# Kernel tuning notes

Hardware: AMD Instinct MI355X
Metric: run time of the kernel (lower is better)

Reference implementation:

```python
import jax, jax.numpy as jnp
import numpy as np

EPS = 1e-3  # Keras BatchNormalization default epsilon


def _bn_params(key, c):
    k1, k2, k3, k4 = jax.random.split(key, 4)
    gamma = 1.0 + 0.1 * jax.random.normal(k1, (c,), jnp.float32)
    beta = 0.1 * jax.random.normal(k2, (c,), jnp.float32)
    mean = 0.1 * jax.random.normal(k3, (c,), jnp.float32)
    var = 0.5 + jax.random.uniform(k4, (c,), jnp.float32)
    return jnp.stack([gamma, beta, mean, var])  # (4, c)


def bn(x, p):
    g, b, m, v = p[0], p[1], p[2], p[3]
    return (x - m) * jax.lax.rsqrt(v + EPS) * g + b


def setup_inputs() -> dict:
    key = jax.random.key(0)
    ks = jax.random.split(key, 32)
    B, N, C, K = 32, 2048, 3, 32
    MLP1, UNITS = 128, 512
    w = lambda k, shp, fan: jax.random.normal(k, shp, jnp.float32) / np.sqrt(fan)
    inp = {
        "inputs": jax.random.normal(ks[0], (B, N, C), jnp.float32),
        "indices": jax.random.randint(ks[1], (B, N, K), 0, N, jnp.int32),
        "t_conv1_w": w(ks[2], (C, 64), C), "t_conv1_b": 0.1 * jax.random.normal(ks[3], (64,), jnp.float32),
        "t_bn1": _bn_params(ks[4], 64),
        "t_dense1_w": w(ks[5], (64, 64), 64), "t_dense1_b": 0.1 * jax.random.normal(ks[6], (64,), jnp.float32),
        "t_bn2": _bn_params(ks[7], 64),
        "t_dense2_w": w(ks[8], (64, C * C), 64), "t_dense2_b": 0.1 * jax.random.normal(ks[9], (C * C,), jnp.float32),
        "conv1_w": w(ks[10], (K * C, MLP1), K * C), "conv1_b": 0.1 * jax.random.normal(ks[11], (MLP1,), jnp.float32),
        "bn1": _bn_params(ks[12], MLP1),
        "conv2_w": w(ks[13], (MLP1, 2 * MLP1), MLP1), "conv2_b": 0.1 * jax.random.normal(ks[14], (2 * MLP1,), jnp.float32),
        "bn2": _bn_params(ks[15], 2 * MLP1),
        "bn3": _bn_params(ks[16], 2 * MLP1),
        "dense1_w": w(ks[17], (2 * MLP1, C), 2 * MLP1), "dense1_b": 0.1 * jax.random.normal(ks[18], (C,), jnp.float32),
        "conv3_w": w(ks[19], (C, UNITS), C), "conv3_b": 0.1 * jax.random.normal(ks[20], (UNITS,), jnp.float32),
        "bn4": _bn_params(ks[21], UNITS),
        "blk1_w": w(ks[22], (UNITS, UNITS // 2), UNITS), "blk1_b": 0.1 * jax.random.normal(ks[23], (UNITS // 2,), jnp.float32),
        "blk1_bn": _bn_params(ks[24], UNITS // 2),
        "blk2_w": w(ks[25], (UNITS // 2, UNITS // 4), UNITS // 2), "blk2_b": 0.1 * jax.random.normal(ks[26], (UNITS // 4,), jnp.float32),
        "blk2_bn": _bn_params(ks[27], UNITS // 4),
        "bn_globf": _bn_params(ks[28], UNITS // 4),
    }
    return inp


def reference(inputs, indices, t_conv1_w, t_conv1_b, t_bn1, t_dense1_w, t_dense1_b,
              t_bn2, t_dense2_w, t_dense2_b, conv1_w, conv1_b, bn1, conv2_w, conv2_b,
              bn2, bn3, dense1_w, dense1_b, conv3_w, conv3_b, bn4,
              blk1_w, blk1_b, blk1_bn, blk2_w, blk2_b, blk2_bn, bn_globf):
    B, N, C = inputs.shape
    # --- TNetLess (inference: dropout = identity) ---
    x = jax.nn.relu(bn(inputs @ t_conv1_w + t_conv1_b, t_bn1))   # (B,N,64)
    x = jnp.max(x, axis=1)                                        # global max pool -> (B,64)
    x = jax.nn.relu(bn(x @ t_dense1_w + t_dense1_b, t_bn2))      # (B,64)
    transform = (x @ t_dense2_w + t_dense2_b).reshape(B, C, C)   # (B,C,C)
    pct = jnp.einsum('bnc,bcd->bnd', inputs, transform)          # transformed cloud (B,N,C)
    # --- random neighbor gather (batch_dims=1) ---
    feats = pct[jnp.arange(B)[:, None, None], indices]           # (B,N,K,C)
    feats = feats.reshape(B, N, -1)                               # (B,N,K*C)
    # --- pointwise MLP over gathered neighbor features ---
    feats = jax.nn.relu(bn(feats @ conv1_w + conv1_b, bn1))      # (B,N,128)
    feats = jax.nn.relu(bn(feats @ conv2_w + conv2_b, bn2))      # (B,N,256)
    g = bn(jnp.max(feats, axis=1), bn3)                           # (B,256)
    g = jnp.broadcast_to(g[:, None, :], (B, N, g.shape[-1]))     # tile to (B,N,256)
    g = g @ dense1_w + dense1_b                                   # (B,N,C)
    combined = jnp.concatenate([pct, g], axis=1)                  # concat on point axis -> (B,2N,C)
    # --- conv3 + conv blocks (kernel_size=1 -> pointwise) ---
    net = jax.nn.relu(bn(combined @ conv3_w + conv3_b, bn4))     # (B,2N,512)
    net = jax.nn.relu(bn(net @ blk1_w + blk1_b, blk1_bn))        # (B,2N,256)
    net = jax.nn.relu(bn(net @ blk2_w + blk2_b, blk2_bn))        # (B,2N,128)
    net = jnp.max(net, axis=1)                                    # (B,128)
    return bn(net, bn_globf)
```

## Files before the change

kernel.cpp:

```cpp
#include <hip/hip_runtime.h>

typedef unsigned short u16;
typedef unsigned int u32;
typedef __attribute__((ext_vector_type(8))) short bf16x8;
typedef __attribute__((ext_vector_type(4))) float f32x4;

#define EPSBN 0.001f
#define MFMA16(a, b, c) __builtin_amdgcn_mfma_f32_16x16x32_bf16(a, b, c, 0, 0, 0)

__device__ __forceinline__ float bf2f(u16 u) {
    return __uint_as_float(((u32)u) << 16);
}
__device__ __forceinline__ u16 f2bf(float f) {
    u32 u = __float_as_uint(f);
    u32 r = u + 0x7FFFu + ((u >> 16) & 1u);
    return (u16)(r >> 16);
}
__device__ __forceinline__ float relu(float x) { return x > 0.f ? x : 0.f; }

#define A_INPUTS 64
#define A_TC1W  196672
#define A_TC1B  196864
#define A_TBN1  196928
#define A_TD1W  197184
#define A_TD1B  201280
#define A_TBN2  201344
#define A_TD2W  201600
#define A_TD2B  202176
#define A_C1W   202240
#define A_C1B   214528
#define A_BN1   214656
#define A_C2W   215168
#define A_C2B   247936
#define A_BN2   248192
#define A_BN3   249216
#define A_D1W   250240
#define A_D1B   251008
#define A_C3W   251072
#define A_C3B   252608
#define A_BN4   253120
#define A_BLK1W 255168
#define A_BLK1B 386240
#define A_BLK1BN 386496
#define A_BLK2W 387520
#define A_BLK2B 420288
#define A_BLK2BN 420416
#define A_BNGF  420928
#define S_TRF   423488
#define S_PCT   423808
#define S_MAXF  620544
#define S_NETMAX 628736
#define S_XMAX  632832
#define T_C1WT  634880
#define T_C2WT  641024
#define T_W4T   657408
#define T_W5T   722944

struct ConvArgs {
    const void* src[28];
    int n[28];
    int off[28];
};

struct PrepArgs {
    const float* src[4];
    u16* dst[4];
    int K[4];
    int logN[4];
    int base[4];
};

__global__ __launch_bounds__(256) void k_convert(ConvArgs a, const u16* __restrict__ tbn1,
                                                 float* __restrict__ ws, u32* __restrict__ flag) {
    int ok = 1;
    for (int i = 0; i < 16; i += 2) {
        u16 v = tbn1[i];
        if (v < 0x3E00u || v > 0x4080u) ok = 0;
    }
    if (blockIdx.x == 0 && blockIdx.y == 0 && threadIdx.x == 0) flag[0] = ok ? 1u : 0u;

    int t = blockIdx.y;
    int n = a.n[t];
    int cpb = (n + 31) >> 5;
    int s = blockIdx.x * cpb;
    int e = s + cpb; if (e > n) e = n;
    float* dst = ws + a.off[t];
    if (ok) {
        const u16* src = (const u16*)a.src[t];
        for (int i = s + (int)threadIdx.x; i < e; i += 256) dst[i] = bf2f(src[i]);
    } else {
        const float* src = (const float*)a.src[t];
        for (int i = s + (int)threadIdx.x; i < e; i += 256) dst[i] = src[i];
    }
}

__global__ __launch_bounds__(256) void k_prepw_all(PrepArgs pa) {
    int blk = blockIdx.x;
    int t = (blk < 48) ? 0 : (blk < 176) ? 1 : (blk < 688) ? 2 : 3;
    int i = (blk - pa.base[t]) * 256 + (int)threadIdx.x;
    int N1 = (1 << pa.logN[t]) - 1;
    int k = i >> pa.logN[t], c = i & N1;
    pa.dst[t][c * pa.K[t] + k] = f2bf(pa.src[t][i]);
}

__global__ __launch_bounds__(256) void k_tnet1(const float* __restrict__ inp,
                                               const float* __restrict__ w,
                                               const float* __restrict__ bias,
                                               const float* __restrict__ bn,
                                               u32* __restrict__ xmax) {
    __shared__ float pts[1536];
    __shared__ float wred[4][64];
    int b = blockIdx.y, slice = blockIdx.x, tid = threadIdx.x;
    const float* ip = inp + ((size_t)b * 2048 + slice * 512) * 3;
#pragma unroll
    for (int i = 0; i < 6; i++) pts[tid + i * 256] = ip[tid + i * 256];

    int c = tid & 63, np = tid >> 6;
    float w0 = w[c], w1 = w[64 + c], w2 = w[128 + c], bi = bias[c];
    float g = bn[c], be = bn[64 + c], m = bn[128 + c], v = bn[192 + c];
    float s = g * rsqrtf(v + EPSBN), t = be - m * s;
    __syncthreads();

    float vmax = 0.f;
    int pbase = np * 128;
#pragma unroll 4
    for (int p = 0; p < 128; p++) {
        float x0 = pts[(pbase + p) * 3], x1 = pts[(pbase + p) * 3 + 1], x2 = pts[(pbase + p) * 3 + 2];
        float z = x0 * w0 + x1 * w1 + x2 * w2 + bi;
        vmax = fmaxf(vmax, z * s + t);
    }
    wred[np][c] = vmax;
    __syncthreads();
    if (tid < 64) {
        float mm = fmaxf(fmaxf(wred[0][tid], wred[1][tid]), fmaxf(wred[2][tid], wred[3][tid]));
        atomicMax(&xmax[b * 64 + tid], __float_as_uint(relu(mm)));
    }
}

__global__ __launch_bounds__(64) void k_tnet2(const float* __restrict__ xmax,
                                              const float* __restrict__ w1, const float* __restrict__ b1,
                                              const float* __restrict__ bn2p,
                                              const float* __restrict__ w2, const float* __restrict__ b2,
                                              float* __restrict__ transform) {
    int b = blockIdx.x, t = threadIdx.x;
    __shared__ float x2[64];
    const float* xm = xmax + b * 64;
    float acc = b1[t];
    for (int j = 0; j < 64; j++) acc += xm[j] * w1[j * 64 + t];
    float g = bn2p[t], be = bn2p[64 + t], m = bn2p[128 + t], v = bn2p[192 + t];
    float s = g * rsqrtf(v + EPSBN);
    x2[t] = relu(acc * s + (be - m * s));
    __syncthreads();
    if (t < 9) {
        float a = b2[t];
        for (int j = 0; j < 64; j++) a += x2[j] * w2[j * 9 + t];
        transform[b * 9 + t] = a;
    }
}

__global__ __launch_bounds__(256) void k_pct(const float* __restrict__ inp,
                                             const float* __restrict__ transform,
                                             float* __restrict__ pct) {
    int b = blockIdx.y;
    int n = blockIdx.x * 256 + threadIdx.x;
    __shared__ float T[9];
    if (threadIdx.x < 9) T[threadIdx.x] = transform[b * 9 + threadIdx.x];
    __syncthreads();
    const float* ip = inp + ((size_t)b * 2048 + n) * 3;
    float x0 = ip[0], x1 = ip[1], x2 = ip[2];
    float* op = pct + ((size_t)b * 2049 + n) * 3;
    op[0] = x0 * T[0] + x1 * T[3] + x2 * T[6];
    op[1] = x0 * T[1] + x1 * T[4] + x2 * T[7];
    op[2] = x0 * T[2] + x1 * T[5] + x2 * T[8];
}

__global__ __launch_bounds__(256) void k_feat(const float* __restrict__ pct,
                                              const int* __restrict__ indices,
                                              const u16* __restrict__ w1t, const float* __restrict__ b1,
                                              const float* __restrict__ bn1p,
                                              const u16* __restrict__ w2t, const float* __restrict__ b2,
                                              const float* __restrict__ bn2p,
                                              u32* __restrict__ maxfeats) {
    __shared__ __align__(16) u16 ftA[4096];
    __shared__ __align__(16) u16 h1B[4096];
    __shared__ float sB1[128], sS1[128], sT1[128];
    __shared__ float sB2[256], sS2[256], sT2[256];

    int b = blockIdx.y, n0p = blockIdx.x * 32, tid = threadIdx.x;
    if (tid < 128) {
        float g = bn1p[tid], be = bn1p[128 + tid], m = bn1p[256 + tid], v = bn1p[384 + tid];
        float s = g * rsqrtf(v + EPSBN);
        sS1[tid] = s; sT1[tid] = be - m * s; sB1[tid] = b1[tid];
    }
    {
        int c = tid;
        float g = bn2p[c], be = bn2p[256 + c], m = bn2p[512 + c], v = bn2p[768 + c];
        float s = g * rsqrtf(v + EPSBN);
        sS2[c] = s; sT2[c] = be - m * s; sB2[c] = b2[c];
    }
    {
        const float* pb = pct + (size_t)b * 2049 * 3;
        const int* ib = indices + ((size_t)b * 2048 + n0p) * 32;
        char* fA = (char*)ftA;
#pragma unroll
        for (int r = 0; r < 4; r++) {
            int i = tid + 256 * r;
            int p = i >> 5, k = i & 31;
            int idx = ib[p * 32 + k];
            const float* s = pb + (size_t)idx * 3;
            int sw = (p & 7) << 4;
            int base = p * 256 + 6 * k;
            *(u16*)(fA + ((base) ^ sw)) = f2bf(s[0]);
            *(u16*)(fA + ((base + 2) ^ sw)) = f2bf(s[1]);
            *(u16*)(fA + ((base + 4) ^ sw)) = f2bf(s[2]);
        }
    }
    __syncthreads();

    int lane = tid & 63, wv = tid >> 6;
    int rw = lane & 15, kq = lane >> 4;
    int axor = (rw & 7) << 4;

    {
        f32x4 acc[2][2];
#pragma unroll
        for (int m = 0; m < 2; m++)
#pragma unroll
            for (int n = 0; n < 2; n++) acc[m][n] = (f32x4){0.f, 0.f, 0.f, 0.f};
        const char* fA = (const char*)ftA;
        const char* W = (const char*)w1t;
        int nb = wv * 32;
#pragma unroll
        for (int ks = 0; ks < 3; ks++) {
            bf16x8 a0 = *(const bf16x8*)(fA + ((rw * 256 + ks * 64 + kq * 16) ^ axor));
            bf16x8 a1 = *(const bf16x8*)(fA + (((rw + 16) * 256 + ks * 64 + kq * 16) ^ axor));
            bf16x8 b0 = *(const bf16x8*)(W + ((nb + rw) * 192 + ks * 64 + kq * 16));
            bf16x8 b1v = *(const bf16x8*)(W + ((nb + 16 + rw) * 192 + ks * 64 + kq * 16));
            acc[0][0] = MFMA16(a0, b0, acc[0][0]);
            acc[1][0] = MFMA16(a1, b0, acc[1][0]);
            acc[0][1] = MFMA16(a0, b1v, acc[0][1]);
            acc[1][1] = MFMA16(a1, b1v, acc[1][1]);
        }
        char* hB = (char*)h1B;
#pragma unroll
        for (int nt = 0; nt < 2; nt++) {
            int c = nb + nt * 16 + rw;
            float s = sS1[c], t = sT1[c], bi = sB1[c];
#pragma unroll
            for (int m = 0; m < 2; m++)
#pragma unroll
                for (int r = 0; r < 4; r++) {
                    int rr = m * 16 + kq * 4 + r;
                    float h = relu((acc[m][nt][r] + bi) * s + t);
                    *(u16*)(hB + ((rr * 256 + c * 2) ^ ((rr & 7) << 4))) = f2bf(h);
                }
        }
    }
    __syncthreads();
    {
        f32x4 acc[2][4];
#pragma unroll
        for (int m = 0; m < 2; m++)
#pragma unroll
            for (int n = 0; n < 4; n++) acc[m][n] = (f32x4){0.f, 0.f, 0.f, 0.f};
        const char* hB = (const char*)h1B;
        const char* W = (const char*)w2t;
        int nb = wv * 64;
#pragma unroll
        for (int ks = 0; ks < 4; ks++) {
            bf16x8 a0 = *(const bf16x8*)(hB + ((rw * 256 + ks * 64 + kq * 16) ^ axor));
            bf16x8 a1 = *(const bf16x8*)(hB + (((rw + 16) * 256 + ks * 64 + kq * 16) ^ axor));
#pragma unroll
            for (int nt = 0; nt < 4; nt++) {
                bf16x8 bv = *(const bf16x8*)(W + ((nb + nt * 16 + rw) * 256 + ks * 64 + kq * 16));
                acc[0][nt] = MFMA16(a0, bv, acc[0][nt]);
                acc[1][nt] = MFMA16(a1, bv, acc[1][nt]);
            }
        }
#pragma unroll
        for (int nt = 0; nt < 4; nt++) {
            int c = nb + nt * 16 + rw;
            float s = sS2[c], t = sT2[c], bi = sB2[c];
            float vm = 0.f;
#pragma unroll
            for (int m = 0; m < 2; m++)
#pragma unroll
                for (int r = 0; r < 4; r++)
                    vm = fmaxf(vm, relu((acc[m][nt][r] + bi) * s + t));
            vm = fmaxf(vm, __shfl_xor(vm, 16));
            vm = fmaxf(vm, __shfl_xor(vm, 32));
            if (kq == 0) atomicMax(&maxfeats[b * 256 + c], __float_as_uint(vm));
        }
    }
}

__global__ __launch_bounds__(256) void k_gvec(const u32* __restrict__ maxfeats,
                                              const float* __restrict__ bn3p,
                                              const float* __restrict__ dw, const float* __restrict__ db,
                                              float* __restrict__ pct) {
    int b = blockIdx.x, c = threadIdx.x;
    __shared__ float red[3][256];
    float mf = __uint_as_float(maxfeats[b * 256 + c]);
    float g = bn3p[c], be = bn3p[256 + c], m = bn3p[512 + c], v = bn3p[768 + c];
    float s = g * rsqrtf(v + EPSBN);
    float y = mf * s + (be - m * s);
    red[0][c] = y * dw[c * 3 + 0];
    red[1][c] = y * dw[c * 3 + 1];
    red[2][c] = y * dw[c * 3 + 2];
    __syncthreads();
    for (int st = 128; st > 0; st >>= 1) {
        if (c < st) {
            red[0][c] += red[0][c + st];
            red[1][c] += red[1][c + st];
            red[2][c] += red[2][c + st];
        }
        __syncthreads();
    }
    if (c < 3) pct[((size_t)b * 2049 + 2048) * 3 + c] = red[c][0] + db[c];
}

__global__ __launch_bounds__(256) void k_mlp(const float* __restrict__ pct,
                                             const float* __restrict__ w3, const float* __restrict__ b3,
                                             const float* __restrict__ bn4p,
                                             const u16* __restrict__ w4t, const float* __restrict__ b4f,
                                             const float* __restrict__ bn5p,
                                             const u16* __restrict__ w5t, const float* __restrict__ b5f,
                                             const float* __restrict__ bn6p,
                                             u32* __restrict__ netmax) {
    __shared__ __align__(16) u16 hA[16384];
    __shared__ __align__(16) u16 hB[8192];
    __shared__ float rowsS[128];
    __shared__ float sB4[256], sS5[256], sT5[256];
    __shared__ float sB5[128], sS6[128], sT6[128];

    int b = blockIdx.y, r0 = blockIdx.x * 32, tid = threadIdx.x;
    int nrows = 2049 - r0; if (nrows > 32) nrows = 32;

    {
        int c = tid;
        float g = bn5p[c], be = bn5p[256 + c], m = bn5p[512 + c], v = bn5p[768 + c];
        float s = g * rsqrtf(v + EPSBN);
        sS5[c] = s; sT5[c] = be - m * s; sB4[c] = b4f[c];
    }
    if (tid < 128) {
        int c = tid;
        float g = bn6p[c], be = bn6p[128 + c], m = bn6p[256 + c], v = bn6p[384 + c];
        float s = g * rsqrtf(v + EPSBN);
        sS6[c] = s; sT6[c] = be - m * s; sB5[c] = b5f[c];
    }
    if (tid < 32) {
        float v0 = 0.f, v1 = 0.f, v2 = 0.f;
        if (tid < nrows) {
            const float* s = pct + ((size_t)b * 2049 + r0 + tid) * 3;
            v0 = s[0]; v1 = s[1]; v2 = s[2];
        }
        rowsS[tid * 4] = v0; rowsS[tid * 4 + 1] = v1; rowsS[tid * 4 + 2] = v2;
    }
    __syncthreads();
    {
        char* hAc = (char*)hA;
#pragma unroll
        for (int half = 0; half < 2; half++) {
            int c = tid + half * 256;
            float w0 = w3[c], w1f = w3[512 + c], w2f = w3[1024 + c];
            float bi = b3[c];
            float g = bn4p[c], be = bn4p[512 + c], m = bn4p[1024 + c], v = bn4p[1536 + c];
            float s = g * rsqrtf(v + EPSBN), t = be - m * s;
#pragma unroll
            for (int p = 0; p < 32; p++) {
                float z = rowsS[p * 4] * w0 + rowsS[p * 4 + 1] * w1f + rowsS[p * 4 + 2] * w2f + bi;
                float h = relu(z * s + t);
                *(u16*)(hAc + ((p * 1024 + c * 2) ^ ((p & 7) << 4))) = f2bf(h);
            }
        }
    }
    __syncthreads();

    int lane = tid & 63, wv = tid >> 6;
    int rw = lane & 15, kq = lane >> 4;
    int axor = (rw & 7) << 4;

    {
        f32x4 acc[2][4];
#pragma unroll
        for (int m = 0; m < 2; m++)
#pragma unroll
            for (int n = 0; n < 4; n++) acc[m][n] = (f32x4){0.f, 0.f, 0.f, 0.f};
        const char* A = (const char*)hA;
        const char* W = (const char*)w4t;
        int nb = wv * 64;
        auto lA = [&](int m, int ks) -> bf16x8 {
            return *(const bf16x8*)(A + (((rw + m) * 1024 + ks * 64 + kq * 16) ^ axor));
        };
        auto lB = [&](int nt, int ks) -> bf16x8 {
            return *(const bf16x8*)(W + ((nb + nt * 16 + rw) * 1024 + ks * 64 + kq * 16));
        };
        bf16x8 a0 = lA(0, 0), a1 = lA(16, 0);
        bf16x8 b0 = lB(0, 0), b1v = lB(1, 0), b2v = lB(2, 0), b3v = lB(3, 0);
#pragma unroll
        for (int ks = 0; ks < 16; ks++) {
            bf16x8 na0, na1, nb0, nb1, nb2, nb3;
            if (ks < 15) {
                na0 = lA(0, ks + 1); na1 = lA(16, ks + 1);
                nb0 = lB(0, ks + 1); nb1 = lB(1, ks + 1); nb2 = lB(2, ks + 1); nb3 = lB(3, ks + 1);
            }
            acc[0][0] = MFMA16(a0, b0, acc[0][0]);  acc[1][0] = MFMA16(a1, b0, acc[1][0]);
            acc[0][1] = MFMA16(a0, b1v, acc[0][1]); acc[1][1] = MFMA16(a1, b1v, acc[1][1]);
            acc[0][2] = MFMA16(a0, b2v, acc[0][2]); acc[1][2] = MFMA16(a1, b2v, acc[1][2]);
            acc[0][3] = MFMA16(a0, b3v, acc[0][3]); acc[1][3] = MFMA16(a1, b3v, acc[1][3]);
            if (ks < 15) { a0 = na0; a1 = na1; b0 = nb0; b1v = nb1; b2v = nb2; b3v = nb3; }
        }
        char* HB = (char*)hB;
#pragma unroll
        for (int nt = 0; nt < 4; nt++) {
            int c = nb + nt * 16 + rw;
            float s = sS5[c], t = sT5[c], bi = sB4[c];
#pragma unroll
            for (int m = 0; m < 2; m++)
#pragma unroll
                for (int r = 0; r < 4; r++) {
                    int rr = m * 16 + kq * 4 + r;
                    float h = relu((acc[m][nt][r] + bi) * s + t);
                    *(u16*)(HB + ((rr * 512 + c * 2) ^ ((rr & 7) << 4))) = f2bf(h);
                }
        }
    }
    __syncthreads();
    {
        f32x4 acc[2][2];
#pragma unroll
        for (int m = 0; m < 2; m++)
#pragma unroll
            for (int n = 0; n < 2; n++) acc[m][n] = (f32x4){0.f, 0.f, 0.f, 0.f};
        const char* A = (const char*)hB;
        const char* W = (const char*)w5t;
        int nb = wv * 32;
#pragma unroll
        for (int ks = 0; ks < 8; ks++) {
            bf16x8 a0 = *(const bf16x8*)(A + ((rw * 512 + ks * 64 + kq * 16) ^ axor));
            bf16x8 a1 = *(const bf16x8*)(A + (((rw + 16) * 512 + ks * 64 + kq * 16) ^ axor));
            bf16x8 w0 = *(const bf16x8*)(W + ((nb + rw) * 512 + ks * 64 + kq * 16));
            bf16x8 w1v = *(const bf16x8*)(W + ((nb + 16 + rw) * 512 + ks * 64 + kq * 16));
            acc[0][0] = MFMA16(a0, w0, acc[0][0]);
            acc[1][0] = MFMA16(a1, w0, acc[1][0]);
            acc[0][1] = MFMA16(a0, w1v, acc[0][1]);
            acc[1][1] = MFMA16(a1, w1v, acc[1][1]);
        }
#pragma unroll
        for (int nt = 0; nt < 2; nt++) {
            int c = nb + nt * 16 + rw;
            float s = sS6[c], t = sT6[c], bi = sB5[c];
            float vm = 0.f;
#pragma unroll
            for (int m = 0; m < 2; m++)
#pragma unroll
                for (int r = 0; r < 4; r++) {
                    int rr = m * 16 + kq * 4 + r;
                    float h = relu((acc[m][nt][r] + bi) * s + t);
                    if (rr < nrows) vm = fmaxf(vm, h);
                }
            vm = fmaxf(vm, __shfl_xor(vm, 16));
            vm = fmaxf(vm, __shfl_xor(vm, 32));
            if (kq == 0) atomicMax(&netmax[b * 128 + c], __float_as_uint(vm));
        }
    }
}

__global__ __launch_bounds__(256) void k_out(const u32* __restrict__ netmax,
                                             const float* __restrict__ bng,
                                             const u32* __restrict__ flag,
                                             void* __restrict__ out) {
    int i = blockIdx.x * 256 + threadIdx.x;
    int c = i & 127;
    float v = __uint_as_float(netmax[i]);
    float g = bng[c], be = bng[128 + c], m = bng[256 + c], va = bng[384 + c];
    float s = g * rsqrtf(va + EPSBN);
    float val = v * s + (be - m * s);
    if (flag[0]) ((u16*)out)[i] = f2bf(val);
    else ((float*)out)[i] = val;
}

extern "C" void kernel_launch(void* const* d_in, const int* in_sizes, int n_in,
                              void* d_out, int out_size, void* d_ws, size_t ws_size,
                              hipStream_t stream) {
    float* ws = (float*)d_ws;
    u32* flag = (u32*)ws;

    static const int order[28] = {0,2,3,4,5,6,7,8,9,10,11,12,13,14,15,16,17,18,19,20,21,22,23,24,25,26,27,28};
    static const int nels[28] = {196608,192,64,256,4096,64,256,576,9,12288,128,512,32768,256,1024,1024,768,3,1536,512,2048,131072,256,1024,32768,128,512,512};
    static const int offs[28] = {A_INPUTS,A_TC1W,A_TC1B,A_TBN1,A_TD1W,A_TD1B,A_TBN2,A_TD2W,A_TD2B,A_C1W,A_C1B,A_BN1,A_C2W,A_C2B,A_BN2,A_BN3,A_D1W,A_D1B,A_C3W,A_C3B,A_BN4,A_BLK1W,A_BLK1B,A_BLK1BN,A_BLK2W,A_BLK2B,A_BLK2BN,A_BNGF};
    ConvArgs ca;
    for (int i = 0; i < 28; i++) { ca.src[i] = d_in[order[i]]; ca.n[i] = nels[i]; ca.off[i] = offs[i]; }

    const int* indices = (const int*)d_in[1];

    k_convert<<<dim3(32, 28), 256, 0, stream>>>(ca, (const u16*)d_in[4], ws, flag);

    PrepArgs pa;
    pa.src[0] = ws + A_C1W;   pa.dst[0] = (u16*)(ws + T_C1WT); pa.K[0] = 96;  pa.logN[0] = 7; pa.base[0] = 0;
    pa.src[1] = ws + A_C2W;   pa.dst[1] = (u16*)(ws + T_C2WT); pa.K[1] = 128; pa.logN[1] = 8; pa.base[1] = 48;
    pa.src[2] = ws + A_BLK1W; pa.dst[2] = (u16*)(ws + T_W4T);  pa.K[2] = 512; pa.logN[2] = 8; pa.base[2] = 176;
    pa.src[3] = ws + A_BLK2W; pa.dst[3] = (u16*)(ws + T_W5T);  pa.K[3] = 256; pa.logN[3] = 7; pa.base[3] = 688;
    k_prepw_all<<<816, 256, 0, stream>>>(pa);

    hipMemsetAsync(ws + S_MAXF, 0, (size_t)14336 * 4, stream);

    k_tnet1<<<dim3(4, 32), 256, 0, stream>>>(ws + A_INPUTS, ws + A_TC1W, ws + A_TC1B, ws + A_TBN1,
                                             (u32*)(ws + S_XMAX));
    k_tnet2<<<32, 64, 0, stream>>>((const float*)(ws + S_XMAX), ws + A_TD1W, ws + A_TD1B, ws + A_TBN2,
                                   ws + A_TD2W, ws + A_TD2B, ws + S_TRF);
    k_pct<<<dim3(8, 32), 256, 0, stream>>>(ws + A_INPUTS, ws + S_TRF, ws + S_PCT);
    k_feat<<<dim3(64, 32), 256, 0, stream>>>(ws + S_PCT, indices,
                                             (const u16*)(ws + T_C1WT), ws + A_C1B, ws + A_BN1,
                                             (const u16*)(ws + T_C2WT), ws + A_C2B, ws + A_BN2,
                                             (u32*)(ws + S_MAXF));
    k_gvec<<<32, 256, 0, stream>>>((u32*)(ws + S_MAXF), ws + A_BN3, ws + A_D1W, ws + A_D1B, ws + S_PCT);
    k_mlp<<<dim3(65, 32), 256, 0, stream>>>(ws + S_PCT,
                                            ws + A_C3W, ws + A_C3B, ws + A_BN4,
                                            (const u16*)(ws + T_W4T), ws + A_BLK1B, ws + A_BLK1BN,
                                            (const u16*)(ws + T_W5T), ws + A_BLK2B, ws + A_BLK2BN,
                                            (u32*)(ws + S_NETMAX));
    k_out<<<16, 256, 0, stream>>>((u32*)(ws + S_NETMAX), ws + A_BNGF, flag, d_out);
}
```

Measured before the change: 271.2 us.

## Fold batchnorm into weights and double row tiles with chunked conv3 pipelining

Batchnorm scale and shift are folded into the bf16 weight transposes and the bias vectors during weight prep, so the MLP epilogues become a bias-add plus relu. k_feat and k_mlp now process 64 rows per block instead of 32, which halves the grid and reuses each weight fragment across four M tiles. In k_mlp the conv3 activations are produced in 64-channel chunks into a double buffer, interleaved with the blk1 MFMA loop, which shrinks LDS and overlaps the VALU work with matrix ops. The risks are higher register pressure under launch_bounds(256,3), a barrier per chunk, and a smaller grid.

```diff
diff --git a/kernel.cpp b/kernel.cpp
--- a/kernel.cpp
+++ b/kernel.cpp
@@ -55,6 +55,12 @@
 #define T_C2WT  641024
 #define T_W4T   657408
 #define T_W5T   722944
+#define P_W3S   739328
+#define P_B3S   740864
+#define P_BP1   741376
+#define P_BP2   741504
+#define P_BP4   741760
+#define P_BP5   742016
 
 struct ConvArgs {
     const void* src[28];
@@ -64,6 +70,7 @@
 
 struct PrepArgs {
     const float* src[4];
+    const float* bn[4];
     u16* dst[4];
     int K[4];
     int logN[4];
@@ -98,9 +105,42 @@
     int blk = blockIdx.x;
     int t = (blk < 48) ? 0 : (blk < 176) ? 1 : (blk < 688) ? 2 : 3;
     int i = (blk - pa.base[t]) * 256 + (int)threadIdx.x;
-    int N1 = (1 << pa.logN[t]) - 1;
-    int k = i >> pa.logN[t], c = i & N1;
-    pa.dst[t][c * pa.K[t] + k] = f2bf(pa.src[t][i]);
+    int N = 1 << pa.logN[t];
+    int k = i >> pa.logN[t], c = i & (N - 1);
+    const float* bn = pa.bn[t];
+    float s = bn[c] * rsqrtf(bn[3 * N + c] + EPSBN);
+    pa.dst[t][c * pa.K[t] + k] = f2bf(pa.src[t][i] * s);
+}
+
+__global__ __launch_bounds__(256) void k_prepsmall(float* __restrict__ ws) {
+    int tid = threadIdx.x;
+    for (int c = tid; c < 512; c += 256) {
+        const float* bn = ws + A_BN4;
+        float s = bn[c] * rsqrtf(bn[1536 + c] + EPSBN);
+        float t = bn[512 + c] - bn[1024 + c] * s;
+        ws[P_W3S + c]        = ws[A_C3W + c] * s;
+        ws[P_W3S + 512 + c]  = ws[A_C3W + 512 + c] * s;
+        ws[P_W3S + 1024 + c] = ws[A_C3W + 1024 + c] * s;
+        ws[P_B3S + c] = ws[A_C3B + c] * s + t;
+    }
+    {
+        int c = tid;
+        const float* bn2 = ws + A_BN2;
+        float s2 = bn2[c] * rsqrtf(bn2[768 + c] + EPSBN);
+        ws[P_BP2 + c] = ws[A_C2B + c] * s2 + (bn2[256 + c] - bn2[512 + c] * s2);
+        const float* bn5 = ws + A_BLK1BN;
+        float s5 = bn5[c] * rsqrtf(bn5[768 + c] + EPSBN);
+        ws[P_BP4 + c] = ws[A_BLK1B + c] * s5 + (bn5[256 + c] - bn5[512 + c] * s5);
+    }
+    if (tid < 128) {
+        int c = tid;
+        const float* bn1 = ws + A_BN1;
+        float s1 = bn1[c] * rsqrtf(bn1[384 + c] + EPSBN);
+        ws[P_BP1 + c] = ws[A_C1B + c] * s1 + (bn1[128 + c] - bn1[256 + c] * s1);
+        const float* bn6 = ws + A_BLK2BN;
+        float s6 = bn6[c] * rsqrtf(bn6[384 + c] + EPSBN);
+        ws[P_BP5 + c] = ws[A_BLK2B + c] * s6 + (bn6[128 + c] - bn6[256 + c] * s6);
+    }
 }
 
 __global__ __launch_bounds__(256) void k_tnet1(const float* __restrict__ inp,
@@ -174,43 +214,31 @@
     op[2] = x0 * T[2] + x1 * T[5] + x2 * T[8];
 }
 
-__global__ __launch_bounds__(256) void k_feat(const float* __restrict__ pct,
-                                              const int* __restrict__ indices,
-                                              const u16* __restrict__ w1t, const float* __restrict__ b1,
-                                              const float* __restrict__ bn1p,
-                                              const u16* __restrict__ w2t, const float* __restrict__ b2,
-                                              const float* __restrict__ bn2p,
-                                              u32* __restrict__ maxfeats) {
-    __shared__ __align__(16) u16 ftA[4096];
-    __shared__ __align__(16) u16 h1B[4096];
-    __shared__ float sB1[128], sS1[128], sT1[128];
-    __shared__ float sB2[256], sS2[256], sT2[256];
-
-    int b = blockIdx.y, n0p = blockIdx.x * 32, tid = threadIdx.x;
-    if (tid < 128) {
-        float g = bn1p[tid], be = bn1p[128 + tid], m = bn1p[256 + tid], v = bn1p[384 + tid];
-        float s = g * rsqrtf(v + EPSBN);
-        sS1[tid] = s; sT1[tid] = be - m * s; sB1[tid] = b1[tid];
-    }
-    {
-        int c = tid;
-        float g = bn2p[c], be = bn2p[256 + c], m = bn2p[512 + c], v = bn2p[768 + c];
-        float s = g * rsqrtf(v + EPSBN);
-        sS2[c] = s; sT2[c] = be - m * s; sB2[c] = b2[c];
-    }
+__global__ __launch_bounds__(256, 3) void k_feat(const float* __restrict__ pct,
+                                                 const int* __restrict__ indices,
+                                                 const u16* __restrict__ w1t, const float* __restrict__ bp1,
+                                                 const u16* __restrict__ w2t, const float* __restrict__ bp2,
+                                                 u32* __restrict__ maxfeats) {
+    __shared__ __align__(16) u16 ftA[8192];
+    __shared__ __align__(16) u16 h1B[8192];
+    __shared__ float sp1[128], sp2[256];
+
+    int b = blockIdx.y, n0p = blockIdx.x * 64, tid = threadIdx.x;
+    sp2[tid] = bp2[tid];
+    if (tid < 128) sp1[tid] = bp1[tid];
     {
         const float* pb = pct + (size_t)b * 2049 * 3;
         const int* ib = indices + ((size_t)b * 2048 + n0p) * 32;
         char* fA = (char*)ftA;
 #pragma unroll
-        for (int r = 0; r < 4; r++) {
+        for (int r = 0; r < 8; r++) {
             int i = tid + 256 * r;
             int p = i >> 5, k = i & 31;
             int idx = ib[p * 32 + k];
             const float* s = pb + (size_t)idx * 3;
             int sw = (p & 7) << 4;
             int base = p * 256 + 6 * k;
-            *(u16*)(fA + ((base) ^ sw)) = f2bf(s[0]);
+            *(u16*)(fA + ((base) ^ sw))     = f2bf(s[0]);
             *(u16*)(fA + ((base + 2) ^ sw)) = f2bf(s[1]);
             *(u16*)(fA + ((base + 4) ^ sw)) = f2bf(s[2]);
         }
@@ -222,71 +250,79 @@
     int axor = (rw & 7) << 4;
 
     {
-        f32x4 acc[2][2];
-#pragma unroll
-        for (int m = 0; m < 2; m++)
+        f32x4 acc[4][2];
+#pragma unroll
+        for (int m = 0; m < 4; m++)
 #pragma unroll
             for (int n = 0; n < 2; n++) acc[m][n] = (f32x4){0.f, 0.f, 0.f, 0.f};
-        const char* fA = (const char*)ftA;
+        const char* A = (const char*)ftA;
         const char* W = (const char*)w1t;
         int nb = wv * 32;
 #pragma unroll
         for (int ks = 0; ks < 3; ks++) {
-            bf16x8 a0 = *(const bf16x8*)(fA + ((rw * 256 + ks * 64 + kq * 16) ^ axor));
-            bf16x8 a1 = *(const bf16x8*)(fA + (((rw + 16) * 256 + ks * 64 + kq * 16) ^ axor));
-            bf16x8 b0 = *(const bf16x8*)(W + ((nb + rw) * 192 + ks * 64 + kq * 16));
-            bf16x8 b1v = *(const bf16x8*)(W + ((nb + 16 + rw) * 192 + ks * 64 + kq * 16));
-            acc[0][0] = MFMA16(a0, b0, acc[0][0]);
-            acc[1][0] = MFMA16(a1, b0, acc[1][0]);
-            acc[0][1] = MFMA16(a0, b1v, acc[0][1]);
-            acc[1][1] = MFMA16(a1, b1v, acc[1][1]);
+            int kb = ks * 64 + kq * 16;
+            bf16x8 b0 = *(const bf16x8*)(W + (nb + rw) * 192 + kb);
+            bf16x8 b1 = *(const bf16x8*)(W + (nb + 16 + rw) * 192 + kb);
+            bf16x8 a0 = *(const bf16x8*)(A + (((rw) * 256 + kb) ^ axor));
+            bf16x8 a1 = *(const bf16x8*)(A + (((rw + 16) * 256 + kb) ^ axor));
+            bf16x8 a2 = *(const bf16x8*)(A + (((rw + 32) * 256 + kb) ^ axor));
+            bf16x8 a3 = *(const bf16x8*)(A + (((rw + 48) * 256 + kb) ^ axor));
+            acc[0][0] = MFMA16(a0, b0, acc[0][0]); acc[0][1] = MFMA16(a0, b1, acc[0][1]);
+            acc[1][0] = MFMA16(a1, b0, acc[1][0]); acc[1][1] = MFMA16(a1, b1, acc[1][1]);
+            acc[2][0] = MFMA16(a2, b0, acc[2][0]); acc[2][1] = MFMA16(a2, b1, acc[2][1]);
+            acc[3][0] = MFMA16(a3, b0, acc[3][0]); acc[3][1] = MFMA16(a3, b1, acc[3][1]);
         }
         char* hB = (char*)h1B;
 #pragma unroll
         for (int nt = 0; nt < 2; nt++) {
             int c = nb + nt * 16 + rw;
-            float s = sS1[c], t = sT1[c], bi = sB1[c];
-#pragma unroll
-            for (int m = 0; m < 2; m++)
+            float bb = sp1[c];
+#pragma unroll
+            for (int m = 0; m < 4; m++)
 #pragma unroll
                 for (int r = 0; r < 4; r++) {
                     int rr = m * 16 + kq * 4 + r;
-                    float h = relu((acc[m][nt][r] + bi) * s + t);
+                    float h = relu(acc[m][nt][r] + bb);
                     *(u16*)(hB + ((rr * 256 + c * 2) ^ ((rr & 7) << 4))) = f2bf(h);
                 }
         }
     }
     __syncthreads();
     {
-        f32x4 acc[2][4];
-#pragma unroll
-        for (int m = 0; m < 2; m++)
+        f32x4 acc[4][4];
+#pragma unroll
+        for (int m = 0; m < 4; m++)
 #pragma unroll
             for (int n = 0; n < 4; n++) acc[m][n] = (f32x4){0.f, 0.f, 0.f, 0.f};
-        const char* hB = (const char*)h1B;
+        const char* A = (const char*)h1B;
         const char* W = (const char*)w2t;
         int nb = wv * 64;
 #pragma unroll
         for (int ks = 0; ks < 4; ks++) {
-            bf16x8 a0 = *(const bf16x8*)(hB + ((rw * 256 + ks * 64 + kq * 16) ^ axor));
-            bf16x8 a1 = *(const bf16x8*)(hB + (((rw + 16) * 256 + ks * 64 + kq * 16) ^ axor));
+            int kb = ks * 64 + kq * 16;
+            bf16x8 a0 = *(const bf16x8*)(A + (((rw) * 256 + kb) ^ axor));
+            bf16x8 a1 = *(const bf16x8*)(A + (((rw + 16) * 256 + kb) ^ axor));
+            bf16x8 a2 = *(const bf16x8*)(A + (((rw + 32) * 256 + kb) ^ axor));
+            bf16x8 a3 = *(const bf16x8*)(A + (((rw + 48) * 256 + kb) ^ axor));
 #pragma unroll
             for (int nt = 0; nt < 4; nt++) {
-                bf16x8 bv = *(const bf16x8*)(W + ((nb + nt * 16 + rw) * 256 + ks * 64 + kq * 16));
+                bf16x8 bv = *(const bf16x8*)(W + (nb + nt * 16 + rw) * 256 + kb);
                 acc[0][nt] = MFMA16(a0, bv, acc[0][nt]);
                 acc[1][nt] = MFMA16(a1, bv, acc[1][nt]);
+                acc[2][nt] = MFMA16(a2, bv, acc[2][nt]);
+                acc[3][nt] = MFMA16(a3, bv, acc[3][nt]);
             }
         }
 #pragma unroll
         for (int nt = 0; nt < 4; nt++) {
             int c = nb + nt * 16 + rw;
-            float s = sS2[c], t = sT2[c], bi = sB2[c];
+            float bb = sp2[c];
             float vm = 0.f;
 #pragma unroll
-            for (int m = 0; m < 2; m++)
+            for (int m = 0; m < 4; m++)
 #pragma unroll
                 for (int r = 0; r < 4; r++)
-                    vm = fmaxf(vm, relu((acc[m][nt][r] + bi) * s + t));
+                    vm = fmaxf(vm, relu(acc[m][nt][r] + bb));
             vm = fmaxf(vm, __shfl_xor(vm, 16));
             vm = fmaxf(vm, __shfl_xor(vm, 32));
             if (kq == 0) atomicMax(&maxfeats[b * 256 + c], __float_as_uint(vm));
@@ -319,117 +355,107 @@
     if (c < 3) pct[((size_t)b * 2049 + 2048) * 3 + c] = red[c][0] + db[c];
 }
 
-__global__ __launch_bounds__(256) void k_mlp(const float* __restrict__ pct,
-                                             const float* __restrict__ w3, const float* __restrict__ b3,
-                                             const float* __restrict__ bn4p,
-                                             const u16* __restrict__ w4t, const float* __restrict__ b4f,
-                                             const float* __restrict__ bn5p,
-                                             const u16* __restrict__ w5t, const float* __restrict__ b5f,
-                                             const float* __restrict__ bn6p,
-                                             u32* __restrict__ netmax) {
-    __shared__ __align__(16) u16 hA[16384];
-    __shared__ __align__(16) u16 hB[8192];
-    __shared__ float rowsS[128];
-    __shared__ float sB4[256], sS5[256], sT5[256];
-    __shared__ float sB5[128], sS6[128], sT6[128];
-
-    int b = blockIdx.y, r0 = blockIdx.x * 32, tid = threadIdx.x;
-    int nrows = 2049 - r0; if (nrows > 32) nrows = 32;
-
-    {
-        int c = tid;
-        float g = bn5p[c], be = bn5p[256 + c], m = bn5p[512 + c], v = bn5p[768 + c];
-        float s = g * rsqrtf(v + EPSBN);
-        sS5[c] = s; sT5[c] = be - m * s; sB4[c] = b4f[c];
-    }
-    if (tid < 128) {
-        int c = tid;
-        float g = bn6p[c], be = bn6p[128 + c], m = bn6p[256 + c], v = bn6p[384 + c];
-        float s = g * rsqrtf(v + EPSBN);
-        sS6[c] = s; sT6[c] = be - m * s; sB5[c] = b5f[c];
-    }
-    if (tid < 32) {
+__global__ __launch_bounds__(256, 3) void k_mlp(const float* __restrict__ pct,
+                                                const float* __restrict__ w3s, const float* __restrict__ b3s,
+                                                const u16* __restrict__ w4t, const float* __restrict__ bp4,
+                                                const u16* __restrict__ w5t, const float* __restrict__ bp5,
+                                                u32* __restrict__ netmax) {
+    __shared__ __align__(16) u16 hA[2][4096];
+    __shared__ __align__(16) u16 hB[16384];
+    __shared__ float rows4[256];
+    __shared__ float sb4[256], sb5[128];
+
+    int b = blockIdx.y, r0 = blockIdx.x * 64, tid = threadIdx.x;
+    int nrows = 2049 - r0; if (nrows > 64) nrows = 64;
+
+    sb4[tid] = bp4[tid];
+    if (tid < 128) sb5[tid] = bp5[tid];
+    if (tid < 64) {
         float v0 = 0.f, v1 = 0.f, v2 = 0.f;
         if (tid < nrows) {
             const float* s = pct + ((size_t)b * 2049 + r0 + tid) * 3;
             v0 = s[0]; v1 = s[1]; v2 = s[2];
         }
-        rowsS[tid * 4] = v0; rowsS[tid * 4 + 1] = v1; rowsS[tid * 4 + 2] = v2;
-    }
-    __syncthreads();
-    {
-        char* hAc = (char*)hA;
-#pragma unroll
-        for (int half = 0; half < 2; half++) {
-            int c = tid + half * 256;
-            float w0 = w3[c], w1f = w3[512 + c], w2f = w3[1024 + c];
-            float bi = b3[c];
-            float g = bn4p[c], be = bn4p[512 + c], m = bn4p[1024 + c], v = bn4p[1536 + c];
-            float s = g * rsqrtf(v + EPSBN), t = be - m * s;
-#pragma unroll
-            for (int p = 0; p < 32; p++) {
-                float z = rowsS[p * 4] * w0 + rowsS[p * 4 + 1] * w1f + rowsS[p * 4 + 2] * w2f + bi;
-                float h = relu(z * s + t);
-                *(u16*)(hAc + ((p * 1024 + c * 2) ^ ((p & 7) << 4))) = f2bf(h);
-            }
-        }
+        rows4[tid * 4] = v0; rows4[tid * 4 + 1] = v1; rows4[tid * 4 + 2] = v2;
     }
     __syncthreads();
 
     int lane = tid & 63, wv = tid >> 6;
     int rw = lane & 15, kq = lane >> 4;
     int axor = (rw & 7) << 4;
+    int chv = tid & 63;
+    int rquart = tid >> 6;
+
+    auto phase1 = [&](int c, int bufi) {
+        int ch = c * 64 + chv;
+        float w0 = w3s[ch], w1 = w3s[512 + ch], w2 = w3s[1024 + ch], bb = b3s[ch];
+        char* dst = (char*)hA[bufi];
+#pragma unroll
+        for (int r = 0; r < 16; r++) {
+            int row = rquart * 16 + r;
+            float x0 = rows4[row * 4], x1 = rows4[row * 4 + 1], x2 = rows4[row * 4 + 2];
+            float h = relu(x0 * w0 + x1 * w1 + x2 * w2 + bb);
+            *(u16*)(dst + ((row * 128 + chv * 2) ^ ((row & 7) << 4))) = f2bf(h);
+        }
+    };
+
+    phase1(0, 0);
+    __syncthreads();
 
     {
-        f32x4 acc[2][4];
-#pragma unroll
-        for (int m = 0; m < 2; m++)
+        f32x4 acc[4][4];
+#pragma unroll
+        for (int m = 0; m < 4; m++)
 #pragma unroll
             for (int n = 0; n < 4; n++) acc[m][n] = (f32x4){0.f, 0.f, 0.f, 0.f};
-        const char* A = (const char*)hA;
         const char* W = (const char*)w4t;
         int nb = wv * 64;
-        auto lA = [&](int m, int ks) -> bf16x8 {
-            return *(const bf16x8*)(A + (((rw + m) * 1024 + ks * 64 + kq * 16) ^ axor));
-        };
-        auto lB = [&](int nt, int ks) -> bf16x8 {
-            return *(const bf16x8*)(W + ((nb + nt * 16 + rw) * 1024 + ks * 64 + kq * 16));
-        };
-        bf16x8 a0 = lA(0, 0), a1 = lA(16, 0);
-        bf16x8 b0 = lB(0, 0), b1v = lB(1, 0), b2v = lB(2, 0), b3v = lB(3, 0);
-#pragma unroll
-        for (int ks = 0; ks < 16; ks++) {
-            bf16x8 na0, na1, nb0, nb1, nb2, nb3;
-            if (ks < 15) {
-                na0 = lA(0, ks + 1); na1 = lA(16, ks + 1);
-                nb0 = lB(0, ks + 1); nb1 = lB(1, ks + 1); nb2 = lB(2, ks + 1); nb3 = lB(3, ks + 1);
+        for (int c = 0; c < 8; c++) {
+            bf16x8 bfr[2][4];
+#pragma unroll
+            for (int ksl = 0; ksl < 2; ksl++)
+#pragma unroll
+                for (int nt = 0; nt < 4; nt++)
+                    bfr[ksl][nt] = *(const bf16x8*)(W + (nb + nt * 16 + rw) * 1024 + c * 128 + ksl * 64 + kq * 16);
+            if (c < 7) phase1(c + 1, (c + 1) & 1);
+            const char* A = (const char*)hA[c & 1];
+#pragma unroll
+            for (int ksl = 0; ksl < 2; ksl++) {
+                int kb = ksl * 64 + kq * 16;
+                bf16x8 a0 = *(const bf16x8*)(A + (((rw) * 128 + kb) ^ axor));
+                bf16x8 a1 = *(const bf16x8*)(A + (((rw + 16) * 128 + kb) ^ axor));
+                bf16x8 a2 = *(const bf16x8*)(A + (((rw + 32) * 128 + kb) ^ axor));
+                bf16x8 a3 = *(const bf16x8*)(A + (((rw + 48) * 128 + kb) ^ axor));
+#pragma unroll
+                for (int nt = 0; nt < 4; nt++) {
+                    acc[0][nt] = MFMA16(a0, bfr[ksl][nt], acc[0][nt]);
+                    acc[1][nt] = MFMA16(a1, bfr[ksl][nt], acc[1][nt]);
+                    acc[2][nt] = MFMA16(a2, bfr[ksl][nt], acc[2][nt]);
+                    acc[3][nt] = MFMA16(a3, bfr[ksl][nt], acc[3][nt]);
+                }
             }
-            acc[0][0] = MFMA16(a0, b0, acc[0][0]);  acc[1][0] = MFMA16(a1, b0, acc[1][0]);
-            acc[0][1] = MFMA16(a0, b1v, acc[0][1]); acc[1][1] = MFMA16(a1, b1v, acc[1][1]);
-            acc[0][2] = MFMA16(a0, b2v, acc[0][2]); acc[1][2] = MFMA16(a1, b2v, acc[1][2]);
-            acc[0][3] = MFMA16(a0, b3v, acc[0][3]); acc[1][3] = MFMA16(a1, b3v, acc[1][3]);
-            if (ks < 15) { a0 = na0; a1 = na1; b0 = nb0; b1v = nb1; b2v = nb2; b3v = nb3; }
+            __syncthreads();
         }
         char* HB = (char*)hB;
 #pragma unroll
         for (int nt = 0; nt < 4; nt++) {
             int c = nb + nt * 16 + rw;
-            float s = sS5[c], t = sT5[c], bi = sB4[c];
-#pragma unroll
-            for (int m = 0; m < 2; m++)
+            float bb = sb4[c];
+#pragma unroll
+            for (int m = 0; m < 4; m++)
 #pragma unroll
                 for (int r = 0; r < 4; r++) {
                     int rr = m * 16 + kq * 4 + r;
-                    float h = relu((acc[m][nt][r] + bi) * s + t);
+                    float h = relu(acc[m][nt][r] + bb);
                     *(u16*)(HB + ((rr * 512 + c * 2) ^ ((rr & 7) << 4))) = f2bf(h);
                 }
         }
     }
     __syncthreads();
     {
-        f32x4 acc[2][2];
-#pragma unroll
-        for (int m = 0; m < 2; m++)
+        f32x4 acc[4][2];
+#pragma unroll
+        for (int m = 0; m < 4; m++)
 #pragma unroll
             for (int n = 0; n < 2; n++) acc[m][n] = (f32x4){0.f, 0.f, 0.f, 0.f};
         const char* A = (const char*)hB;
@@ -437,26 +463,29 @@
         int nb = wv * 32;
 #pragma unroll
         for (int ks = 0; ks < 8; ks++) {
-            bf16x8 a0 = *(const bf16x8*)(A + ((rw * 512 + ks * 64 + kq * 16) ^ axor));
-            bf16x8 a1 = *(const bf16x8*)(A + (((rw + 16) * 512 + ks * 64 + kq * 16) ^ axor));
-            bf16x8 w0 = *(const bf16x8*)(W + ((nb + rw) * 512 + ks * 64 + kq * 16));
-            bf16x8 w1v = *(const bf16x8*)(W + ((nb + 16 + rw) * 512 + ks * 64 + kq * 16));
-            acc[0][0] = MFMA16(a0, w0, acc[0][0]);
-            acc[1][0] = MFMA16(a1, w0, acc[1][0]);
-            acc[0][1] = MFMA16(a0, w1v, acc[0][1]);
-            acc[1][1] = MFMA16(a1, w1v, acc[1][1]);
+            int kb = ks * 64 + kq * 16;
+            bf16x8 b0 = *(const bf16x8*)(W + (nb + rw) * 512 + kb);
+            bf16x8 b1 = *(const bf16x8*)(W + (nb + 16 + rw) * 512 + kb);
+            bf16x8 a0 = *(const bf16x8*)(A + (((rw) * 512 + kb) ^ axor));
+            bf16x8 a1 = *(const bf16x8*)(A + (((rw + 16) * 512 + kb) ^ axor));
+            bf16x8 a2 = *(const bf16x8*)(A + (((rw + 32) * 512 + kb) ^ axor));
+            bf16x8 a3 = *(const bf16x8*)(A + (((rw + 48) * 512 + kb) ^ axor));
+            acc[0][0] = MFMA16(a0, b0, acc[0][0]); acc[0][1] = MFMA16(a0, b1, acc[0][1]);
+            acc[1][0] = MFMA16(a1, b0, acc[1][0]); acc[1][1] = MFMA16(a1, b1, acc[1][1]);
+            acc[2][0] = MFMA16(a2, b0, acc[2][0]); acc[2][1] = MFMA16(a2, b1, acc[2][1]);
+            acc[3][0] = MFMA16(a3, b0, acc[3][0]); acc[3][1] = MFMA16(a3, b1, acc[3][1]);
         }
 #pragma unroll
         for (int nt = 0; nt < 2; nt++) {
             int c = nb + nt * 16 + rw;
-            float s = sS6[c], t = sT6[c], bi = sB5[c];
+            float bb = sb5[c];
             float vm = 0.f;
 #pragma unroll
-            for (int m = 0; m < 2; m++)
+            for (int m = 0; m < 4; m++)
 #pragma unroll
                 for (int r = 0; r < 4; r++) {
                     int rr = m * 16 + kq * 4 + r;
-                    float h = relu((acc[m][nt][r] + bi) * s + t);
+                    float h = relu(acc[m][nt][r] + bb);
                     if (rr < nrows) vm = fmaxf(vm, h);
                 }
             vm = fmaxf(vm, __shfl_xor(vm, 16));
@@ -497,11 +526,12 @@
     k_convert<<<dim3(32, 28), 256, 0, stream>>>(ca, (const u16*)d_in[4], ws, flag);
 
     PrepArgs pa;
-    pa.src[0] = ws + A_C1W;   pa.dst[0] = (u16*)(ws + T_C1WT); pa.K[0] = 96;  pa.logN[0] = 7; pa.base[0] = 0;
-    pa.src[1] = ws + A_C2W;   pa.dst[1] = (u16*)(ws + T_C2WT); pa.K[1] = 128; pa.logN[1] = 8; pa.base[1] = 48;
-    pa.src[2] = ws + A_BLK1W; pa.dst[2] = (u16*)(ws + T_W4T);  pa.K[2] = 512; pa.logN[2] = 8; pa.base[2] = 176;
-    pa.src[3] = ws + A_BLK2W; pa.dst[3] = (u16*)(ws + T_W5T);  pa.K[3] = 256; pa.logN[3] = 7; pa.base[3] = 688;
+    pa.src[0] = ws + A_C1W;   pa.bn[0] = ws + A_BN1;    pa.dst[0] = (u16*)(ws + T_C1WT); pa.K[0] = 96;  pa.logN[0] = 7; pa.base[0] = 0;
+    pa.src[1] = ws + A_C2W;   pa.bn[1] = ws + A_BN2;    pa.dst[1] = (u16*)(ws + T_C2WT); pa.K[1] = 128; pa.logN[1] = 8; pa.base[1] = 48;
+    pa.src[2] = ws + A_BLK1W; pa.bn[2] = ws + A_BLK1BN; pa.dst[2] = (u16*)(ws + T_W4T);  pa.K[2] = 512; pa.logN[2] = 8; pa.base[2] = 176;
+    pa.src[3] = ws + A_BLK2W; pa.bn[3] = ws + A_BLK2BN; pa.dst[3] = (u16*)(ws + T_W5T);  pa.K[3] = 256; pa.logN[3] = 7; pa.base[3] = 688;
     k_prepw_all<<<816, 256, 0, stream>>>(pa);
+    k_prepsmall<<<1, 256, 0, stream>>>(ws);
 
     hipMemsetAsync(ws + S_MAXF, 0, (size_t)14336 * 4, stream);
 
@@ -510,15 +540,15 @@
     k_tnet2<<<32, 64, 0, stream>>>((const float*)(ws + S_XMAX), ws + A_TD1W, ws + A_TD1B, ws + A_TBN2,
                                    ws + A_TD2W, ws + A_TD2B, ws + S_TRF);
     k_pct<<<dim3(8, 32), 256, 0, stream>>>(ws + A_INPUTS, ws + S_TRF, ws + S_PCT);
-    k_feat<<<dim3(64, 32), 256, 0, stream>>>(ws + S_PCT, indices,
-                                             (const u16*)(ws + T_C1WT), ws + A_C1B, ws + A_BN1,
-                                             (const u16*)(ws + T_C2WT), ws + A_C2B, ws + A_BN2,
+    k_feat<<<dim3(32, 32), 256, 0, stream>>>(ws + S_PCT, indices,
+                                             (const u16*)(ws + T_C1WT), ws + P_BP1,
+                                             (const u16*)(ws + T_C2WT), ws + P_BP2,
                                              (u32*)(ws + S_MAXF));
     k_gvec<<<32, 256, 0, stream>>>((u32*)(ws + S_MAXF), ws + A_BN3, ws + A_D1W, ws + A_D1B, ws + S_PCT);
-    k_mlp<<<dim3(65, 32), 256, 0, stream>>>(ws + S_PCT,
-                                            ws + A_C3W, ws + A_C3B, ws + A_BN4,
-                                            (const u16*)(ws + T_W4T), ws + A_BLK1B, ws + A_BLK1BN,
-                                            (const u16*)(ws + T_W5T), ws + A_BLK2B, ws + A_BLK2BN,
+    k_mlp<<<dim3(33, 32), 256, 0, stream>>>(ws + S_PCT,
+                                            ws + P_W3S, ws + P_B3S,
+                                            (const u16*)(ws + T_W4T), ws + P_BP4,
+                                            (const u16*)(ws + T_W5T), ws + P_BP5,
                                             (u32*)(ws + S_NETMAX));
     k_out<<<16, 256, 0, stream>>>((u32*)(ws + S_NETMAX), ws + A_BNGF, flag, d_out);
 }
```

After: 223.8 us. -17.5%, faster.
